# Kernel optimization log

Measured on AMD Instinct MI355X. Metric: run time of the kernel, lower is better.

## Reference

```python
import jax, jax.numpy as jnp
import numpy as np
import math

LOG_EPS = -1000.0   # matches LOG_EPS in the torch source
NEG = -1e9          # stand-in for -inf (grad-safe)
T_MIN, T_MAX = 0.1, 1.0
GUMBEL_RATIO = 0.5  # gumbel_temperature_ratio forward arg (scalar float)


def setup_inputs() -> dict:
    key = jax.random.key(0)
    k1, k2, k3 = jax.random.split(key, 3)
    B, I, J, D = 4, 96, 384, 256
    return {
        "text_embeddings": jax.random.normal(k1, (B, I, D), jnp.float32),
        "mel_embeddings": jax.random.normal(k2, (B, J, D), jnp.float32),
        "gumbel_noise_u": jax.random.uniform(k3, (B, I, J), jnp.float32,
                                             minval=1e-6, maxval=1.0 - 1e-6),
        "text_mask": jnp.ones((B, I), dtype=bool),
        "mel_mask": jnp.ones((B, J), dtype=bool),
    }


def _soft_alignment(text_embeddings, mel_embeddings, gumbel_noise_u, text_mask, mel_mask):
    B, I, Dt = text_embeddings.shape
    _, J, Dm = mel_embeddings.shape

    # energy (B, I, J) = bmm / sqrt(D_text * D_mel)
    energy = jnp.einsum('bid,bjd->bij', text_embeddings, mel_embeddings) / math.sqrt(Dt * Dm)
    # gumbel noise + temperature
    temperature = T_MIN + (T_MAX - T_MIN) * GUMBEL_RATIO
    noise = -jnp.log(-jnp.log(gumbel_noise_u))
    energy = (energy + noise) / temperature

    len_t = text_mask.sum(1)  # (B,)
    len_m = mel_mask.sum(1)   # (B,)
    j_idx = jnp.arange(J)

    # invalid triangular mask (B, I, J, K): boundary j must not precede previous boundary k
    tri = j_idx[:, None] < j_idx[None, :]                       # (J, K)
    invalid = (tri[None, None]
               | ~text_mask[:, :, None, None]
               | ~mel_mask[:, None, :, None]
               | ~mel_mask[:, None, None, :])
    # force_assign_last: last text token's boundary forced to the last mel frame
    last_i = jnp.arange(I)[None, :] == (len_t - 1)[:, None]     # (B, I)
    not_last_j = j_idx[None, :] != (len_m - 1)[:, None]         # (B, J)
    invalid = invalid | (last_i[:, :, None, None] & not_last_j[:, None, :, None])

    # log conditional prob P(B_i = j | B_{i-1} = k), normalized over j (axis=2)
    e4 = jnp.where(invalid, LOG_EPS, energy[..., None])         # (B, I, J, K)
    log_cond_prob = e4 - jax.nn.logsumexp(e4, axis=2, keepdims=True)
    # reverse logcumsumexp over j: log P(B_i >= j | B_{i-1} = k)
    geq = jnp.flip(jax.lax.cumlogsumexp(jnp.flip(log_cond_prob, 2), axis=2), 2)
    geq = jnp.where(invalid, LOG_EPS, geq)

    # forward DP: B_ij (B, I+1, J+1), B_ij[:,0,0] = 0
    row0 = jnp.full((B, J + 1), NEG).at[:, 0].set(0.0)
    jj = jnp.arange(1, J + 1)

    def step(prev, inp):
        i, lcp = inp                                            # lcp: (B, J, K=J)
        # B_ij[b,i,j] = lse_k B_ij[b,i-1,k] + log_cond_prob[b,i-1,j-1,k]
        vals = jax.nn.logsumexp(prev[:, None, :-1] + lcp, axis=2)  # (B, J)
        window = (jj >= i) & (jj <= J - I + i + 1)              # only j in [i, J-I+i+1] written
        new = jnp.where(window[None, :], vals, NEG)
        new = jnp.concatenate([jnp.full((B, 1), NEG), new], axis=1)
        return new, new

    _, rows = jax.lax.scan(step, row0,
                           (jnp.arange(1, I + 1), jnp.swapaxes(log_cond_prob, 0, 1)))
    Bij = jnp.concatenate([row0[:, None, :], jnp.swapaxes(rows, 0, 1)], axis=1)  # (B, I+1, J+1)

    prob = Bij[:, :-1, :-1]                                     # (B, I, K)
    # log P(B_{i-1} < j <= B_i) = lse_k prob[b,i,k] + geq[b,i,j,k]
    log_boundary = jax.nn.logsumexp(prob[:, :, None, :] + geq, axis=3)  # (B, I, J)
    return log_boundary


def reference(text_embeddings, mel_embeddings, gumbel_noise_u, text_mask, mel_mask):
    soft = _soft_alignment(text_embeddings, mel_embeddings, gumbel_noise_u,
                           text_mask, mel_mask)
    # expanded text embeddings (B, J, D_text)
    expanded = jnp.einsum('bij,bid->bjd', jnp.exp(soft), text_embeddings)
    return soft, expanded
```

## Files before the change

kernel.cpp:

```cpp
#include <hip/hip_runtime.h>
#include <hip/hip_fp16.h>
#include <math.h>

#define B_ 4
#define I_ 96
#define J_ 384
#define D_ 256
#define NEG_     -1000000000.0f
#define NEGINF_  -3.0e38f
#define INV_TEMP_ (1.0f/0.55f)
#define LOG2E_   1.4426950408889634f
#define LN2_     0.6931471805599453f
#define LOGEPS2_ (-1000.0f*LOG2E_)

__device__ __forceinline__ float lse2(float a, float b) {
    float m = fmaxf(a, b);
    float d = fminf(a, b) - m;
    return m + __log2f(1.0f + __builtin_exp2f(d));
}

template<int CTRL, int RMASK = 0xF>
__device__ __forceinline__ float dpp_id(float x) {
    return __int_as_float(__builtin_amdgcn_update_dpp(
        __float_as_int(NEGINF_), __float_as_int(x), CTRL, RMASK, 0xF, false));
}
__device__ __forceinline__ float rdlane(float x, int l_const) {
    return __int_as_float(__builtin_amdgcn_readlane(__float_as_int(x), l_const));
}

__device__ __forceinline__ float wave_incl_prefix_lse(float x) {
    x = lse2(x, dpp_id<0x111>(x));
    x = lse2(x, dpp_id<0x112>(x));
    x = lse2(x, dpp_id<0x114>(x));
    x = lse2(x, dpp_id<0x118>(x));
    x = lse2(x, dpp_id<0x142, 0xa>(x));
    x = lse2(x, dpp_id<0x143, 0xc>(x));
    return x;
}
__device__ __forceinline__ float wave_incl_suffix_lse(float x, int lane) {
    x = lse2(x, dpp_id<0x101>(x));
    x = lse2(x, dpp_id<0x102>(x));
    x = lse2(x, dpp_id<0x104>(x));
    x = lse2(x, dpp_id<0x108>(x));
    float t1 = rdlane(x, 16), t2 = rdlane(x, 32), t3 = rdlane(x, 48);
    int row = lane >> 4;
    float u23 = lse2(t2, t3);
    float add = (row == 3) ? NEGINF_ : (row == 2) ? t3
              : (row == 1) ? u23 : lse2(t1, u23);
    return lse2(x, add);
}
__device__ __forceinline__ float combine_pre(const float* p, int w) {
    float l01 = lse2(p[0], p[1]);
    float l23 = lse2(p[2], p[3]);
    float P3 = lse2(l01, p[2]);
    float P4 = lse2(l01, l23);
    float P5 = lse2(P4, p[4]);
    return (w == 0) ? NEGINF_ : (w == 1) ? p[0] : (w == 2) ? l01
         : (w == 3) ? P3 : (w == 4) ? P4 : P5;
}
__device__ __forceinline__ float combine_suf(const float* s, int w) {
    float h45 = lse2(s[4], s[5]);
    float h23 = lse2(s[2], s[3]);
    float S3 = lse2(s[3], h45);
    float S2 = lse2(h23, h45);
    float S1 = lse2(s[1], S2);
    return (w == 5) ? NEGINF_ : (w == 4) ? s[5] : (w == 3) ? h45
         : (w == 2) ? S3 : (w == 1) ? S2 : S1;
}

__global__ __launch_bounds__(384) void k_energy(
    const float* __restrict__ text, const float* __restrict__ mel,
    const float* __restrict__ gum, float* __restrict__ Sarr,
    float* __restrict__ Earr)
{
    const int ib = blockIdx.x * 6, b = blockIdx.y;
    const int tid = threadIdx.x, lane = tid & 63, w = tid >> 6;
    __shared__ float4 tex4[6][D_/4];
    __shared__ float e2l[6][J_];

    {
        int r = tid >> 6, c = tid & 63;
        tex4[r][c] = ((const float4*)(text + ((size_t)b*I_ + ib + r)*D_))[c];
    }
    __syncthreads();

    const int j = tid;
    const float4* mrow = (const float4*)(mel + ((size_t)b*J_ + j)*D_);
    float acc[6] = {0.f,0.f,0.f,0.f,0.f,0.f};
    #pragma unroll 4
    for (int d4 = 0; d4 < D_/4; ++d4) {
        float4 m4 = mrow[d4];
        #pragma unroll
        for (int r = 0; r < 6; ++r) {
            float4 t4 = tex4[r][d4];
            acc[r] += t4.x*m4.x + t4.y*m4.y + t4.z*m4.z + t4.w*m4.w;
        }
    }
    #pragma unroll
    for (int r = 0; r < 6; ++r) {
        float u = gum[((size_t)b*I_ + ib + r)*J_ + j];
        float noise = -__logf(-__logf(u));
        e2l[r][j] = (acc[r] * (1.0f/256.0f) + noise) * (INV_TEMP_ * LOG2E_);
    }
    __syncthreads();

    const int k0 = lane * 6;
    float x[6];
    #pragma unroll
    for (int t = 0; t < 6; ++t) x[t] = e2l[w][k0 + t];
    float s1[6], s2[6], sfx[6];
    #pragma unroll
    for (int t = 0; t < 5; ++t) s1[t] = lse2(x[t], x[t+1]);
    s1[5] = x[5];
    #pragma unroll
    for (int t = 0; t < 4; ++t) s2[t] = lse2(s1[t], s1[t+2]);
    s2[4] = s1[4]; s2[5] = s1[5];
    sfx[0] = lse2(s2[0], s2[4]);
    sfx[1] = lse2(s2[1], s2[5]);
    #pragma unroll
    for (int t = 2; t < 6; ++t) sfx[t] = s2[t];
    float incl = wave_incl_suffix_lse(sfx[0], lane);
    float excl = dpp_id<0x130>(incl);
    size_t rowoff = ((size_t)b*I_ + ib + w)*J_ + k0;
    #pragma unroll
    for (int t = 0; t < 6; ++t) {
        Sarr[rowoff + t] = lse2(sfx[t], excl);
        Earr[rowoff + t] = x[t];
    }
}

__global__ __launch_bounds__(384) void k_dp(
    const float* __restrict__ Sarr, const float* __restrict__ Earr,
    float* __restrict__ prob)
{
    __shared__ unsigned int SE[I_*J_];
    const int b = blockIdx.x;
    const int tid = threadIdx.x;
    const float* Sb = Sarr + (size_t)b*I_*J_;
    const float* Eb = Earr + (size_t)b*I_*J_;
    float* Pb = prob + (size_t)b*I_*J_;

    {
        const int k = tid, km1 = (k == 0) ? 0 : k - 1;
        #pragma unroll 4
        for (int r = 0; r < I_; ++r) {
            float s = Sb[(size_t)r*J_ + k];
            float e = Eb[(size_t)r*J_ + km1];
            unsigned int u = ((unsigned int)__half_as_ushort(__float2half(e)) << 16)
                           |  (unsigned int)__half_as_ushort(__float2half(s));
            SE[r*J_ + k] = u;
        }
    }
    __syncthreads();
    if (tid >= 64) return;

    const int lane = tid, k0 = lane * 6;
    float prev[6];
    #pragma unroll
    for (int t = 0; t < 6; ++t) {
        int k = k0 + t;
        float v0 = (k == 0) ? 0.0f : NEG_;
        prev[t] = v0;
        Pb[k] = v0;
    }
    uint2 ca, cb, cc;
    {
        const uint2* p = (const uint2*)&SE[k0];
        ca = p[0]; cb = p[1]; cc = p[2];
    }
    for (int i = 1; i <= I_-1; ++i) {
        const uint2* pn = (const uint2*)&SE[(size_t)i*J_ + k0];
        uint2 na = pn[0], nb = pn[1], nc = pn[2];
        unsigned int uw[6] = { ca.x, ca.y, cb.x, cb.y, cc.x, cc.y };
        float v[6], E6[6];
        #pragma unroll
        for (int t = 0; t < 6; ++t) {
            float S = __half2float(__ushort_as_half((unsigned short)(uw[t] & 0xffff)));
            E6[t]   = __half2float(__ushort_as_half((unsigned short)(uw[t] >> 16)));
            v[t] = prev[t] - S;
        }
        float p1[6], p2[6], p[6];
        p1[0] = v[0];
        #pragma unroll
        for (int t = 1; t < 6; ++t) p1[t] = lse2(v[t-1], v[t]);
        p2[0] = p1[0]; p2[1] = p1[1];
        #pragma unroll
        for (int t = 2; t < 6; ++t) p2[t] = lse2(p1[t-2], p1[t]);
        p[0] = p2[0]; p[1] = p2[1]; p[2] = p2[2]; p[3] = p2[3];
        p[4] = lse2(p2[0], p2[4]);
        p[5] = lse2(p2[1], p2[5]);
        float inc = wave_incl_prefix_lse(p[5]);
        float pexcl = dpp_id<0x138>(inc);
        float nv[6];
        nv[0] = pexcl + E6[0];
        #pragma unroll
        for (int t = 1; t < 6; ++t) nv[t] = lse2(pexcl, p[t-1]) + E6[t];
        float* Prow = Pb + (size_t)i*J_;
        #pragma unroll
        for (int t = 0; t < 6; ++t) {
            int k = k0 + t;
            bool win = (k >= i) && (k <= 289 + i);
            float val = win ? nv[t] : NEG_;
            prev[t] = val;
            Prow[k] = val;
        }
        ca = na; cb = nb; cc = nc;
    }
}

__global__ __launch_bounds__(384) void k_soft(
    float* __restrict__ probsoft,
    const float* __restrict__ Sarr)
{
    const int i = blockIdx.x, b = blockIdx.y;
    const int tid = threadIdx.x, lane = tid & 63, w = tid >> 6;
    const int j = tid;
    __shared__ float tot[12];
    float* Row = probsoft + ((size_t)b*I_ + i)*J_;
    float p = Row[j];

    if (i == I_-1) {
        float sincl = wave_incl_suffix_lse(p, lane);
        if (lane == 0) tot[w] = sincl;
        __syncthreads();
        float m = tot[0];
        #pragma unroll
        for (int t = 1; t < 6; ++t) m = lse2(m, tot[t]);
        Row[j] = (j == J_-1) ? LN2_ * m : LN2_ * m - 1000.0f;
        return;
    }

    float S6 = Sarr[((size_t)b*I_ + i)*J_ + j];
    float v = p - S6;
    float qincl = wave_incl_prefix_lse(v);
    float tsuf  = wave_incl_suffix_lse(p, lane);
    if (lane == 63) tot[w] = qincl;
    if (lane == 0)  tot[6 + w] = tsuf;
    __syncthreads();
    float pt[6], st[6];
    #pragma unroll
    for (int t = 0; t < 6; ++t) { pt[t] = tot[t]; st[t] = tot[6+t]; }
    float Qful = lse2(combine_pre(pt, w), qincl);
    float Texw = dpp_id<0x130>(tsuf);
    float Texc = lse2(combine_suf(st, w), Texw);
    Row[j] = LN2_ * lse2(Qful + S6, Texc + LOGEPS2_);
}

__global__ __launch_bounds__(256) void k_expand(
    const float* __restrict__ soft, const float* __restrict__ text,
    float* __restrict__ out2)
{
    const int jb = blockIdx.x * 8, b = blockIdx.y;
    const int tid = threadIdx.x;
    __shared__ float wsh[8][I_];
    for (int n = tid; n < 8*I_; n += 256) {
        int jj = n / I_, ii = n % I_;
        wsh[jj][ii] = __expf(soft[((size_t)b*I_ + ii)*J_ + jb + jj]);
    }
    __syncthreads();
    float acc[8] = {0.f,0.f,0.f,0.f,0.f,0.f,0.f,0.f};
    const float* tcol = text + (size_t)b*I_*D_ + tid;
    #pragma unroll 4
    for (int ii = 0; ii < I_; ++ii) {
        float tv = tcol[(size_t)ii*D_];
        #pragma unroll
        for (int jj = 0; jj < 8; ++jj) acc[jj] += wsh[jj][ii] * tv;
    }
    #pragma unroll
    for (int jj = 0; jj < 8; ++jj)
        out2[((size_t)b*J_ + jb + jj)*D_ + tid] = acc[jj];
}

extern "C" void kernel_launch(void* const* d_in, const int* in_sizes, int n_in,
                              void* d_out, int out_size, void* d_ws, size_t ws_size,
                              hipStream_t stream) {
    const float* text = (const float*)d_in[0];
    const float* mel  = (const float*)d_in[1];
    const float* gum  = (const float*)d_in[2];

    float* out    = (float*)d_out;
    float* soft   = out;
    float* out2   = out + (size_t)B_*I_*J_;
    float* Sarr   = out2;
    float* Earr   = out2 + (size_t)B_*I_*J_;
    float* prob   = soft;

    k_energy<<<dim3(I_/6, B_), 384, 0, stream>>>(text, mel, gum, Sarr, Earr);
    k_dp    <<<dim3(B_),       384, 0, stream>>>(Sarr, Earr, prob);
    k_soft  <<<dim3(I_, B_),   384, 0, stream>>>(prob, Sarr);
    k_expand<<<dim3(J_/8, B_), 256, 0, stream>>>(soft, text, out2);
}
```

Baseline: 169.9 us.

## Use (max,scale) pair log-sum-exp in DP scan and stream rows from global

```diff
diff --git a/kernel.cpp b/kernel.cpp
--- a/kernel.cpp
+++ b/kernel.cpp
@@ -1,5 +1,5 @@
 #include <hip/hip_runtime.h>
-#include <hip/hip_fp16.h>
+#include <hip/hip_bf16.h>
 #include <math.h>
 
 #define B_ 4
@@ -20,12 +20,31 @@
 }
 
 template<int CTRL, int RMASK = 0xF>
-__device__ __forceinline__ float dpp_id(float x) {
+__device__ __forceinline__ float dpp_mv(float x, float fill) {
     return __int_as_float(__builtin_amdgcn_update_dpp(
-        __float_as_int(NEGINF_), __float_as_int(x), CTRL, RMASK, 0xF, false));
-}
+        __float_as_int(fill), __float_as_int(x), CTRL, RMASK, 0xF, false));
+}
+template<int CTRL, int RMASK = 0xF>
+__device__ __forceinline__ float dpp_id(float x) { return dpp_mv<CTRL,RMASK>(x, NEGINF_); }
 __device__ __forceinline__ float rdlane(float x, int l_const) {
     return __int_as_float(__builtin_amdgcn_readlane(__float_as_int(x), l_const));
+}
+
+__device__ __forceinline__ void pcomb(float& m, float& s, float om, float os) {
+    float d  = om - m;
+    float e  = __builtin_exp2f(-__builtin_fabsf(d));
+    float sh = (d > 0.0f) ? os : s;
+    float sl = (d > 0.0f) ? s  : os;
+    s = __builtin_fmaf(sl, e, sh);
+    m = fmaxf(m, om);
+}
+__device__ __forceinline__ void wave_prefix_pair(float& m, float& s) {
+    { float om=dpp_mv<0x111>(m,NEGINF_), os=dpp_mv<0x111>(s,0.f); pcomb(m,s,om,os); }
+    { float om=dpp_mv<0x112>(m,NEGINF_), os=dpp_mv<0x112>(s,0.f); pcomb(m,s,om,os); }
+    { float om=dpp_mv<0x114>(m,NEGINF_), os=dpp_mv<0x114>(s,0.f); pcomb(m,s,om,os); }
+    { float om=dpp_mv<0x118>(m,NEGINF_), os=dpp_mv<0x118>(s,0.f); pcomb(m,s,om,os); }
+    { float om=dpp_mv<0x142,0xa>(m,NEGINF_), os=dpp_mv<0x142,0xa>(s,0.f); pcomb(m,s,om,os); }
+    { float om=dpp_mv<0x143,0xc>(m,NEGINF_), os=dpp_mv<0x143,0xc>(s,0.f); pcomb(m,s,om,os); }
 }
 
 __device__ __forceinline__ float wave_incl_prefix_lse(float x) {
@@ -129,32 +148,17 @@
     }
 }
 
-__global__ __launch_bounds__(384) void k_dp(
+__global__ __launch_bounds__(64) void k_dp(
     const float* __restrict__ Sarr, const float* __restrict__ Earr,
     float* __restrict__ prob)
 {
-    __shared__ unsigned int SE[I_*J_];
     const int b = blockIdx.x;
-    const int tid = threadIdx.x;
+    const int lane = threadIdx.x;
+    const int k0 = lane * 6;
     const float* Sb = Sarr + (size_t)b*I_*J_;
     const float* Eb = Earr + (size_t)b*I_*J_;
     float* Pb = prob + (size_t)b*I_*J_;
 
-    {
-        const int k = tid, km1 = (k == 0) ? 0 : k - 1;
-        #pragma unroll 4
-        for (int r = 0; r < I_; ++r) {
-            float s = Sb[(size_t)r*J_ + k];
-            float e = Eb[(size_t)r*J_ + km1];
-            unsigned int u = ((unsigned int)__half_as_ushort(__float2half(e)) << 16)
-                           |  (unsigned int)__half_as_ushort(__float2half(s));
-            SE[r*J_ + k] = u;
-        }
-    }
-    __syncthreads();
-    if (tid >= 64) return;
-
-    const int lane = tid, k0 = lane * 6;
     float prev[6];
     #pragma unroll
     for (int t = 0; t < 6; ++t) {
@@ -163,38 +167,57 @@
         prev[t] = v0;
         Pb[k] = v0;
     }
-    uint2 ca, cb, cc;
-    {
-        const uint2* p = (const uint2*)&SE[k0];
-        ca = p[0]; cb = p[1]; cc = p[2];
-    }
-    for (int i = 1; i <= I_-1; ++i) {
-        const uint2* pn = (const uint2*)&SE[(size_t)i*J_ + k0];
-        uint2 na = pn[0], nb = pn[1], nc = pn[2];
-        unsigned int uw[6] = { ca.x, ca.y, cb.x, cb.y, cc.x, cc.y };
+    float SA[6], EA[6], SBf[6], EBf[6];
+    #pragma unroll
+    for (int t = 0; t < 6; ++t) {
+        int k = k0 + t;
+        SA[t] = Sb[k];
+        EA[t] = Eb[(k == 0) ? 0 : k - 1];
+    }
+    #pragma unroll
+    for (int t = 0; t < 6; ++t) {
+        int k = k0 + t;
+        SBf[t] = Sb[(size_t)1*J_ + k];
+        EBf[t] = Eb[(size_t)1*J_ + ((k == 0) ? 0 : k - 1)];
+    }
+
+    auto STEP = [&](int i, float* Sx, float* Ex, int loadrow) {
         float v[6], E6[6];
         #pragma unroll
-        for (int t = 0; t < 6; ++t) {
-            float S = __half2float(__ushort_as_half((unsigned short)(uw[t] & 0xffff)));
-            E6[t]   = __half2float(__ushort_as_half((unsigned short)(uw[t] >> 16)));
-            v[t] = prev[t] - S;
+        for (int t = 0; t < 6; ++t) { v[t] = prev[t] - Sx[t]; E6[t] = Ex[t]; }
+        if (loadrow >= 0) {
+            #pragma unroll
+            for (int t = 0; t < 6; ++t) {
+                int k = k0 + t;
+                Sx[t] = Sb[(size_t)loadrow*J_ + k];
+                Ex[t] = Eb[(size_t)loadrow*J_ + ((k == 0) ? 0 : k - 1)];
+            }
         }
-        float p1[6], p2[6], p[6];
-        p1[0] = v[0];
-        #pragma unroll
-        for (int t = 1; t < 6; ++t) p1[t] = lse2(v[t-1], v[t]);
-        p2[0] = p1[0]; p2[1] = p1[1];
-        #pragma unroll
-        for (int t = 2; t < 6; ++t) p2[t] = lse2(p1[t-2], p1[t]);
-        p[0] = p2[0]; p[1] = p2[1]; p[2] = p2[2]; p[3] = p2[3];
-        p[4] = lse2(p2[0], p2[4]);
-        p[5] = lse2(p2[1], p2[5]);
-        float inc = wave_incl_prefix_lse(p[5]);
-        float pexcl = dpp_id<0x138>(inc);
+        float qm[6], qs[6];
+        qm[0] = v[0]; qs[0] = 1.0f;
+        #pragma unroll
+        for (int t = 1; t < 6; ++t) { qm[t] = v[t]; qs[t] = 1.0f; pcomb(qm[t], qs[t], v[t-1], 1.0f); }
+        float rm[6], rs[6];
+        rm[0] = qm[0]; rs[0] = qs[0]; rm[1] = qm[1]; rs[1] = qs[1];
+        #pragma unroll
+        for (int t = 2; t < 6; ++t) { rm[t] = qm[t]; rs[t] = qs[t]; pcomb(rm[t], rs[t], qm[t-2], qs[t-2]); }
+        float fm[6], fs[6];
+        #pragma unroll
+        for (int t = 0; t < 4; ++t) { fm[t] = rm[t]; fs[t] = rs[t]; }
+        fm[4] = rm[4]; fs[4] = rs[4]; pcomb(fm[4], fs[4], rm[0], rs[0]);
+        fm[5] = rm[5]; fs[5] = rs[5]; pcomb(fm[5], fs[5], rm[1], rs[1]);
+        float Lm = fm[5], Ls = fs[5];
+        wave_prefix_pair(Lm, Ls);
+        float pexm = dpp_mv<0x138>(Lm, NEGINF_);
+        float pexs = dpp_mv<0x138>(Ls, 0.0f);
         float nv[6];
-        nv[0] = pexcl + E6[0];
-        #pragma unroll
-        for (int t = 1; t < 6; ++t) nv[t] = lse2(pexcl, p[t-1]) + E6[t];
+        nv[0] = pexm + __log2f(pexs) + E6[0];
+        #pragma unroll
+        for (int t = 1; t < 6; ++t) {
+            float cm = pexm, cs = pexs;
+            pcomb(cm, cs, fm[t-1], fs[t-1]);
+            nv[t] = cm + __log2f(cs) + E6[t];
+        }
         float* Prow = Pb + (size_t)i*J_;
         #pragma unroll
         for (int t = 0; t < 6; ++t) {
@@ -204,8 +227,14 @@
             prev[t] = val;
             Prow[k] = val;
         }
-        ca = na; cb = nb; cc = nc;
-    }
+    };
+
+    int i = 1;
+    for (; i + 1 <= I_-1; i += 2) {
+        STEP(i,     SA,  EA,  (i + 1 <= I_-2) ? i + 1 : -1);
+        STEP(i + 1, SBf, EBf, (i + 2 <= I_-2) ? i + 2 : -1);
+    }
+    if (i == I_-1) STEP(i, SA, EA, -1);
 }
 
 __global__ __launch_bounds__(384) void k_soft(
@@ -286,7 +315,7 @@
     float* prob   = soft;
 
     k_energy<<<dim3(I_/6, B_), 384, 0, stream>>>(text, mel, gum, Sarr, Earr);
-    k_dp    <<<dim3(B_),       384, 0, stream>>>(Sarr, Earr, prob);
+    k_dp    <<<dim3(B_),        64, 0, stream>>>(Sarr, Earr, prob);
     k_soft  <<<dim3(I_, B_),   384, 0, stream>>>(prob, Sarr);
     k_expand<<<dim3(J_/8, B_), 256, 0, stream>>>(soft, text, out2);
 }
```

New measurement: 163.6 us. 1.04x faster.

## Stream DP rows through double-buffered LDS in a single-wave k_dp

Applied to the files above, without the earlier changes.

```diff
diff --git a/kernel.cpp b/kernel.cpp
--- a/kernel.cpp
+++ b/kernel.cpp
@@ -1,5 +1,5 @@
 #include <hip/hip_runtime.h>
-#include <hip/hip_fp16.h>
+#include <hip/hip_bf16.h>
 #include <math.h>
 
 #define B_ 4
@@ -129,82 +129,100 @@
     }
 }
 
-__global__ __launch_bounds__(384) void k_dp(
+__global__ __launch_bounds__(64) void k_dp(
     const float* __restrict__ Sarr, const float* __restrict__ Earr,
     float* __restrict__ prob)
 {
-    __shared__ unsigned int SE[I_*J_];
+    __shared__ float SEl[2][2][J_];
+    __shared__ float stg[2][J_];
     const int b = blockIdx.x;
-    const int tid = threadIdx.x;
+    const int l = threadIdx.x;
+    const int k0 = l * 6;
     const float* Sb = Sarr + (size_t)b*I_*J_;
     const float* Eb = Earr + (size_t)b*I_*J_;
     float* Pb = prob + (size_t)b*I_*J_;
 
+    #pragma unroll
+    for (int c = 0; c < 6; ++c) { int j = c*64 + l; Pb[j] = (j == 0) ? 0.0f : NEG_; }
+    float prev[6];
+    #pragma unroll
+    for (int t = 0; t < 6; ++t) prev[t] = (k0 + t == 0) ? 0.0f : NEG_;
+
+    float SA[6], EA[6];
+    float sr[6], er[6];
     {
-        const int k = tid, km1 = (k == 0) ? 0 : k - 1;
-        #pragma unroll 4
-        for (int r = 0; r < I_; ++r) {
-            float s = Sb[(size_t)r*J_ + k];
-            float e = Eb[(size_t)r*J_ + km1];
-            unsigned int u = ((unsigned int)__half_as_ushort(__float2half(e)) << 16)
-                           |  (unsigned int)__half_as_ushort(__float2half(s));
-            SE[r*J_ + k] = u;
-        }
-    }
-    __syncthreads();
-    if (tid >= 64) return;
-
-    const int lane = tid, k0 = lane * 6;
-    float prev[6];
-    #pragma unroll
-    for (int t = 0; t < 6; ++t) {
-        int k = k0 + t;
-        float v0 = (k == 0) ? 0.0f : NEG_;
-        prev[t] = v0;
-        Pb[k] = v0;
-    }
-    uint2 ca, cb, cc;
-    {
-        const uint2* p = (const uint2*)&SE[k0];
-        ca = p[0]; cb = p[1]; cc = p[2];
-    }
+        float s0[6], e0[6];
+        #pragma unroll
+        for (int c = 0; c < 6; ++c) {
+            int j = c*64 + l;
+            s0[c] = Sb[j];
+            e0[c] = Eb[(j == 0) ? 0 : j - 1];
+        }
+        #pragma unroll
+        for (int c = 0; c < 6; ++c) {
+            int j = c*64 + l;
+            SEl[0][0][j] = s0[c]; SEl[0][1][j] = e0[c];
+        }
+        __builtin_amdgcn_s_waitcnt(0);
+        #pragma unroll
+        for (int t = 0; t < 6; ++t) { SA[t] = SEl[0][0][k0+t]; EA[t] = SEl[0][1][k0+t]; }
+    }
+    #pragma unroll
+    for (int c = 0; c < 6; ++c) {
+        int j = c*64 + l;
+        sr[c] = Sb[(size_t)1*J_ + j];
+        er[c] = Eb[(size_t)1*J_ + ((j == 0) ? 0 : j - 1)];
+    }
+
     for (int i = 1; i <= I_-1; ++i) {
-        const uint2* pn = (const uint2*)&SE[(size_t)i*J_ + k0];
-        uint2 na = pn[0], nb = pn[1], nc = pn[2];
-        unsigned int uw[6] = { ca.x, ca.y, cb.x, cb.y, cc.x, cc.y };
-        float v[6], E6[6];
-        #pragma unroll
-        for (int t = 0; t < 6; ++t) {
-            float S = __half2float(__ushort_as_half((unsigned short)(uw[t] & 0xffff)));
-            E6[t]   = __half2float(__ushort_as_half((unsigned short)(uw[t] >> 16)));
-            v[t] = prev[t] - S;
-        }
-        float p1[6], p2[6], p[6];
-        p1[0] = v[0];
-        #pragma unroll
-        for (int t = 1; t < 6; ++t) p1[t] = lse2(v[t-1], v[t]);
-        p2[0] = p1[0]; p2[1] = p1[1];
-        #pragma unroll
-        for (int t = 2; t < 6; ++t) p2[t] = lse2(p1[t-2], p1[t]);
-        p[0] = p2[0]; p[1] = p2[1]; p[2] = p2[2]; p[3] = p2[3];
-        p[4] = lse2(p2[0], p2[4]);
-        p[5] = lse2(p2[1], p2[5]);
+        const int par = i & 1;
+        float v[6];
+        #pragma unroll
+        for (int t = 0; t < 6; ++t) v[t] = prev[t] - SA[t];
+        float p[6];
+        p[0] = v[0];
+        #pragma unroll
+        for (int t = 1; t < 6; ++t) p[t] = lse2(p[t-1], v[t]);
         float inc = wave_incl_prefix_lse(p[5]);
         float pexcl = dpp_id<0x138>(inc);
         float nv[6];
-        nv[0] = pexcl + E6[0];
-        #pragma unroll
-        for (int t = 1; t < 6; ++t) nv[t] = lse2(pexcl, p[t-1]) + E6[t];
-        float* Prow = Pb + (size_t)i*J_;
+        nv[0] = pexcl + EA[0];
+        #pragma unroll
+        for (int t = 1; t < 6; ++t) nv[t] = lse2(pexcl, p[t-1]) + EA[t];
+
+        if (i < I_-1) {
+            #pragma unroll
+            for (int c = 0; c < 6; ++c) {
+                int j = c*64 + l;
+                SEl[par][0][j] = sr[c]; SEl[par][1][j] = er[c];
+            }
+            #pragma unroll
+            for (int t = 0; t < 6; ++t) { SA[t] = SEl[par][0][k0+t]; EA[t] = SEl[par][1][k0+t]; }
+            if (i + 1 < I_-1) {
+                #pragma unroll
+                for (int c = 0; c < 6; ++c) {
+                    int j = c*64 + l;
+                    sr[c] = Sb[(size_t)(i+1)*J_ + j];
+                    er[c] = Eb[(size_t)(i+1)*J_ + ((j == 0) ? 0 : j - 1)];
+                }
+            }
+        }
+
+        float val[6];
         #pragma unroll
         for (int t = 0; t < 6; ++t) {
             int k = k0 + t;
             bool win = (k >= i) && (k <= 289 + i);
-            float val = win ? nv[t] : NEG_;
-            prev[t] = val;
-            Prow[k] = val;
-        }
-        ca = na; cb = nb; cc = nc;
+            val[t] = win ? nv[t] : NEG_;
+            prev[t] = val[t];
+        }
+        #pragma unroll
+        for (int t = 0; t < 6; ++t) stg[par][k0 + t] = val[t];
+        #pragma unroll
+        for (int c = 0; c < 6; ++c) {
+            int j = c*64 + l;
+            Pb[(size_t)i*J_ + j] = stg[par][j];
+        }
     }
 }
 
@@ -286,7 +304,7 @@
     float* prob   = soft;
 
     k_energy<<<dim3(I_/6, B_), 384, 0, stream>>>(text, mel, gum, Sarr, Earr);
-    k_dp    <<<dim3(B_),       384, 0, stream>>>(Sarr, Earr, prob);
+    k_dp    <<<dim3(B_),        64, 0, stream>>>(Sarr, Earr, prob);
     k_soft  <<<dim3(I_, B_),   384, 0, stream>>>(prob, Sarr);
     k_expand<<<dim3(J_/8, B_), 256, 0, stream>>>(soft, text, out2);
 }
```

Result: faster. 164.8 us (-3.0%).
